# Performance work log

Measured on AMD Instinct MI355X. Metric: run time of the kernel, lower is better.

Reference implementation:

```python
import jax, jax.numpy as jnp
import numpy as np

N = 100000   # nodes
DIM = 128    # feature dim
E = 800000   # edges per hop
K = 4        # hops
BN_EPS = 1e-5


def setup_inputs() -> dict:
    key = jax.random.key(0)
    ks = jax.random.split(key, 24)
    inp = {}
    for i in range(K):
        inp[f"x{i}"] = jax.random.normal(ks[i], (N, DIM), dtype=jnp.float32)
    inp["edge_attr"] = jax.random.normal(ks[4], (E, DIM), dtype=jnp.float32)
    for i in range(K):
        inp[f"e{i}"] = jax.random.randint(ks[5 + i], (2, E), 0, N, dtype=jnp.int32)
    s1 = 1.0 / np.sqrt(DIM)
    s2 = 1.0 / np.sqrt(2 * DIM)
    inp["W1"] = jax.random.uniform(ks[9], (DIM, 2 * DIM), jnp.float32, -s1, s1)
    inp["b1"] = jax.random.uniform(ks[10], (2 * DIM,), jnp.float32, -s1, s1)
    inp["bn1_g"] = jnp.ones((2 * DIM,), jnp.float32)
    inp["bn1_b"] = jnp.zeros((2 * DIM,), jnp.float32)
    inp["W2"] = jax.random.uniform(ks[11], (2 * DIM, DIM), jnp.float32, -s2, s2)
    inp["b2"] = jax.random.uniform(ks[12], (DIM,), jnp.float32, -s2, s2)
    inp["bn2_g"] = jnp.ones((DIM,), jnp.float32)
    inp["bn2_b"] = jnp.zeros((DIM,), jnp.float32)
    inp["bn3_g"] = jnp.ones((DIM,), jnp.float32)
    inp["bn3_b"] = jnp.zeros((DIM,), jnp.float32)
    inp["eps_param"] = jnp.zeros((K + 1, DIM), jnp.float32)  # nn.Parameter(zeros)
    return inp


def _bn(h, g, b):
    # BatchNorm1d, train-mode math: batch mean / biased var per feature
    m = jnp.mean(h, axis=0)
    v = jnp.var(h, axis=0)
    return g * (h - m) * jax.lax.rsqrt(v + BN_EPS) + b


def _propagate(x, edge_index, edge_attr):
    # message: relu(x_j [+ edge_attr]); aggregate: scatter-add at dst
    msg = x[edge_index[0]]                      # [E, DIM] gather from src
    if edge_attr is not None:
        msg = msg + edge_attr
    msg = jax.nn.relu(msg)
    return jax.ops.segment_sum(msg, edge_index[1], num_segments=N)


def reference(x0, x1, x2, x3, edge_attr, e0, e1, e2, e3,
              W1, b1, bn1_g, bn1_b, W2, b2, bn2_g, bn2_b,
              bn3_g, bn3_b, eps_param):
    xs = [x0, x1, x2, x3]
    es = [e0, e1, e2, e3]
    result = (1.0 + eps_param[0]) * x0
    for i in range(K):
        ea = edge_attr if i == 0 else None
        result = result + (1.0 + eps_param[i + 1]) * _propagate(xs[i], es[i], ea)
    # GIN MLP: Linear -> BN -> ReLU -> Linear -> BN -> ReLU
    h = jax.nn.relu(_bn(result @ W1 + b1, bn1_g, bn1_b))
    h = jax.nn.relu(_bn(h @ W2 + b2, bn2_g, bn2_b))
    # outer ConvBlock: BN -> act (relu, not last layer); dropout in eval = identity
    h = jax.nn.relu(_bn(h, bn3_g, bn3_b))
    return h  # new x[0]; original also carries XX through unchanged
```

## Files before the change

### kernel.cpp

```cpp
#include <hip/hip_runtime.h>
#include <cstdint>
#include <cstddef>

#define NN 100000
#define D 128
#define NE 800000
#define BN_EPS 1e-5f

#define M4 (4 * NN)
#define CH 1000
#define NB 400

__global__ __launch_bounds__(256) void k_count(
    const int* __restrict__ e0, const int* __restrict__ e1,
    const int* __restrict__ e2, const int* __restrict__ e3,
    int* __restrict__ counts) {
  const int h = blockIdx.y;
  const int* e = h == 0 ? e0 : h == 1 ? e1 : h == 2 ? e2 : e3;
  const int eid = blockIdx.x * 256 + threadIdx.x;
  const int dst = e[NE + eid];
  atomicAdd(&counts[dst * 4 + h], 1);
}

__global__ __launch_bounds__(256) void k_scanA(const int* __restrict__ counts,
                                               int* __restrict__ bsum) {
  __shared__ int red[256];
  const int b = blockIdx.x, t = threadIdx.x;
  int s = 0;
  for (int i = t; i < CH; i += 256) s += counts[b * CH + i];
  red[t] = s; __syncthreads();
  for (int off = 128; off > 0; off >>= 1) {
    if (t < off) red[t] += red[t + off];
    __syncthreads();
  }
  if (t == 0) bsum[b] = red[0];
}

__global__ __launch_bounds__(512) void k_scanB(const int* __restrict__ bsum,
                                               int* __restrict__ bpre) {
  __shared__ int s[512];
  const int t = threadIdx.x;
  const int v = (t < NB) ? bsum[t] : 0;
  s[t] = v; __syncthreads();
  for (int off = 1; off < 512; off <<= 1) {
    int x = s[t];
    if (t >= off) x += s[t - off];
    __syncthreads(); s[t] = x; __syncthreads();
  }
  if (t < NB) bpre[t] = s[t] - v;
}

__global__ __launch_bounds__(256) void k_scanC(const int* __restrict__ counts,
                                               const int* __restrict__ bpre,
                                               int* __restrict__ offsets,
                                               int* __restrict__ cursor) {
  __shared__ int cnt[CH];
  __shared__ int part[256];
  const int b = blockIdx.x, t = threadIdx.x;
  for (int i = t; i < CH; i += 256) cnt[i] = counts[b * CH + i];
  __syncthreads();
  int own = 0;
#pragma unroll
  for (int j = 0; j < 4; j++) {
    int idx = t * 4 + j;
    if (idx < CH) own += cnt[idx];
  }
  part[t] = own; __syncthreads();
  for (int off = 1; off < 256; off <<= 1) {
    int x = part[t];
    if (t >= off) x += part[t - off];
    __syncthreads(); part[t] = x; __syncthreads();
  }
  int run = bpre[b] + part[t] - own;
#pragma unroll
  for (int j = 0; j < 4; j++) {
    int idx = t * 4 + j;
    if (idx < CH) {
      offsets[b * CH + idx] = run;
      cursor[b * CH + idx] = run;
      run += cnt[idx];
    }
  }
  if (b == 0 && t == 0) offsets[M4] = 4 * NE;
}

__global__ __launch_bounds__(256) void k_fill(
    const int* __restrict__ e0, const int* __restrict__ e1,
    const int* __restrict__ e2, const int* __restrict__ e3,
    int* __restrict__ cursor, int* __restrict__ srcs, int* __restrict__ eids) {
  const int h = blockIdx.y;
  const int* e = h == 0 ? e0 : h == 1 ? e1 : h == 2 ? e2 : e3;
  const int eid = blockIdx.x * 256 + threadIdx.x;
  const int src = e[eid];
  const int dst = e[NE + eid];
  const int pos = atomicAdd(&cursor[dst * 4 + h], 1);
  srcs[pos] = src;
  if (h == 0) eids[pos] = eid;
}

__global__ __launch_bounds__(256) void k_gather(
    const float* __restrict__ x0, const float* __restrict__ x1,
    const float* __restrict__ x2, const float* __restrict__ x3,
    const float* __restrict__ edge_attr, const float* __restrict__ eps,
    const int* __restrict__ offsets, const int* __restrict__ srcs,
    const int* __restrict__ eids, float* __restrict__ result) {
  const int dst  = blockIdx.x * 4 + (threadIdx.x >> 6);
  const int lane = threadIdx.x & 63;
  const int d    = lane * 2;

  const int4 ob = *reinterpret_cast<const int4*>(offsets + 4 * dst);
  const int o0 = ob.x, b1 = ob.y, b2 = ob.z, b3 = ob.w;
  const int o4 = offsets[4 * dst + 4];

  float2 h0 = make_float2(0.f, 0.f);
  float2 h1 = make_float2(0.f, 0.f);
  float2 h2 = make_float2(0.f, 0.f);
  float2 h3 = make_float2(0.f, 0.f);

  {
    int j = o0;
    for (; j + 2 <= b1; j += 2) {
      const int p0 = srcs[j],     p1 = srcs[j + 1];
      const int q0 = eids[j],     q1 = eids[j + 1];
      float2 v0 = *reinterpret_cast<const float2*>(x0 + p0 * D + d);
      float2 w0 = *reinterpret_cast<const float2*>(edge_attr + (size_t)q0 * D + d);
      float2 v1 = *reinterpret_cast<const float2*>(x0 + p1 * D + d);
      float2 w1 = *reinterpret_cast<const float2*>(edge_attr + (size_t)q1 * D + d);
      h0.x += fmaxf(v0.x + w0.x, 0.f); h0.y += fmaxf(v0.y + w0.y, 0.f);
      h0.x += fmaxf(v1.x + w1.x, 0.f); h0.y += fmaxf(v1.y + w1.y, 0.f);
    }
    if (j < b1) {
      const int p = srcs[j];
      const int q = eids[j];
      float2 v = *reinterpret_cast<const float2*>(x0 + p * D + d);
      float2 w = *reinterpret_cast<const float2*>(edge_attr + (size_t)q * D + d);
      h0.x += fmaxf(v.x + w.x, 0.f); h0.y += fmaxf(v.y + w.y, 0.f);
    }
  }

#define HOP_LOOP(XP, ACC, BEG, END) do {                                       \
    int j_ = (BEG);                                                            \
    for (; j_ + 4 <= (END); j_ += 4) {                                         \
      const int p0_ = srcs[j_], p1_ = srcs[j_ + 1];                            \
      const int p2_ = srcs[j_ + 2], p3_ = srcs[j_ + 3];                        \
      float2 v0_ = *reinterpret_cast<const float2*>((XP) + p0_ * D + d);       \
      float2 v1_ = *reinterpret_cast<const float2*>((XP) + p1_ * D + d);       \
      float2 v2_ = *reinterpret_cast<const float2*>((XP) + p2_ * D + d);       \
      float2 v3_ = *reinterpret_cast<const float2*>((XP) + p3_ * D + d);       \
      ACC.x += fmaxf(v0_.x, 0.f); ACC.y += fmaxf(v0_.y, 0.f);                  \
      ACC.x += fmaxf(v1_.x, 0.f); ACC.y += fmaxf(v1_.y, 0.f);                  \
      ACC.x += fmaxf(v2_.x, 0.f); ACC.y += fmaxf(v2_.y, 0.f);                  \
      ACC.x += fmaxf(v3_.x, 0.f); ACC.y += fmaxf(v3_.y, 0.f);                  \
    }                                                                          \
    for (; j_ < (END); ++j_) {                                                 \
      const int p_ = srcs[j_];                                                 \
      float2 v_ = *reinterpret_cast<const float2*>((XP) + p_ * D + d);         \
      ACC.x += fmaxf(v_.x, 0.f); ACC.y += fmaxf(v_.y, 0.f);                    \
    }                                                                          \
  } while (0)

  HOP_LOOP(x1, h1, b1, b2);
  HOP_LOOP(x2, h2, b2, b3);
  HOP_LOOP(x3, h3, b3, o4);
#undef HOP_LOOP

  float2 e0v = *reinterpret_cast<const float2*>(eps + d);
  float2 s1 = *reinterpret_cast<const float2*>(eps + 1 * D + d);
  float2 s2 = *reinterpret_cast<const float2*>(eps + 2 * D + d);
  float2 s3 = *reinterpret_cast<const float2*>(eps + 3 * D + d);
  float2 s4 = *reinterpret_cast<const float2*>(eps + 4 * D + d);
  float2 xv = *reinterpret_cast<const float2*>(x0 + dst * D + d);

  float2 acc;
  acc.x = (1.f + e0v.x) * xv.x + (1.f + s1.x) * h0.x + (1.f + s2.x) * h1.x
        + (1.f + s3.x) * h2.x + (1.f + s4.x) * h3.x;
  acc.y = (1.f + e0v.y) * xv.y + (1.f + s1.y) * h0.y + (1.f + s2.y) * h1.y
        + (1.f + s3.y) * h2.y + (1.f + s4.y) * h3.y;

  *reinterpret_cast<float2*>(result + dst * D + d) = acc;
}

__global__ __launch_bounds__(512) void k_gemm1(const float* __restrict__ A,
                                               const float* __restrict__ B,
                                               float* __restrict__ C,
                                               float* __restrict__ sums1,
                                               float* __restrict__ sumsq1) {
  __shared__ float As[32][132];
  __shared__ float Bs[32][256];
  const int tid = threadIdx.x;
  const int tx = tid & 31, ty = tid >> 5;
  const int row0 = blockIdx.x * 128;

  float acc[8][8];
#pragma unroll
  for (int i = 0; i < 8; i++)
#pragma unroll
    for (int j = 0; j < 8; j++) acc[i][j] = 0.f;

  for (int k0 = 0; k0 < 128; k0 += 32) {
#pragma unroll
    for (int l = 0; l < 2; l++) {
      int f4 = tid + l * 512;
      int row = f4 >> 3, kq = f4 & 7;
      float4 v = make_float4(0.f, 0.f, 0.f, 0.f);
      if (row0 + row < NN)
        v = *reinterpret_cast<const float4*>(A + (size_t)(row0 + row) * 128 + k0 + kq * 4);
      As[kq * 4 + 0][row] = v.x; As[kq * 4 + 1][row] = v.y;
      As[kq * 4 + 2][row] = v.z; As[kq * 4 + 3][row] = v.w;
    }
#pragma unroll
    for (int l = 0; l < 4; l++) {
      int f4 = tid + l * 512;
      int kk = f4 >> 6, cq = f4 & 63;
      *reinterpret_cast<float4*>(&Bs[kk][cq * 4]) =
          *reinterpret_cast<const float4*>(B + (size_t)(k0 + kk) * 256 + cq * 4);
    }
    __syncthreads();
#pragma unroll
    for (int k = 0; k < 32; k++) {
      float a[8], b[8];
      *reinterpret_cast<float4*>(a)     = *reinterpret_cast<const float4*>(&As[k][ty * 8]);
      *reinterpret_cast<float4*>(a + 4) = *reinterpret_cast<const float4*>(&As[k][ty * 8 + 4]);
      *reinterpret_cast<float4*>(b)     = *reinterpret_cast<const float4*>(&Bs[k][tx * 4]);
      *reinterpret_cast<float4*>(b + 4) = *reinterpret_cast<const float4*>(&Bs[k][128 + tx * 4]);
#pragma unroll
      for (int i = 0; i < 8; i++)
#pragma unroll
        for (int j = 0; j < 8; j++) acc[i][j] = fmaf(a[i], b[j], acc[i][j]);
    }
    __syncthreads();
  }
#pragma unroll
  for (int i = 0; i < 8; i++) {
    int row = row0 + ty * 8 + i;
    if (row < NN) {
      *reinterpret_cast<float4*>(C + (size_t)row * 256 + tx * 4) =
          make_float4(acc[i][0], acc[i][1], acc[i][2], acc[i][3]);
      *reinterpret_cast<float4*>(C + (size_t)row * 256 + 128 + tx * 4) =
          make_float4(acc[i][4], acc[i][5], acc[i][6], acc[i][7]);
    }
  }
  float cs[8], cq[8];
#pragma unroll
  for (int j = 0; j < 8; j++) { cs[j] = 0.f; cq[j] = 0.f; }
#pragma unroll
  for (int i = 0; i < 8; i++)
#pragma unroll
    for (int j = 0; j < 8; j++) { cs[j] += acc[i][j]; cq[j] = fmaf(acc[i][j], acc[i][j], cq[j]); }
#pragma unroll
  for (int j = 0; j < 4; j++) {
    Bs[ty][tx * 4 + j]            = cs[j];
    Bs[16 + ty][tx * 4 + j]       = cq[j];
    Bs[ty][128 + tx * 4 + j]      = cs[4 + j];
    Bs[16 + ty][128 + tx * 4 + j] = cq[4 + j];
  }
  __syncthreads();
  if (tid < 256) {
    float s = 0.f, q = 0.f;
#pragma unroll
    for (int t = 0; t < 16; t++) { s += Bs[t][tid]; q += Bs[16 + t][tid]; }
    unsafeAtomicAdd(&sums1[tid], s);
    unsafeAtomicAdd(&sumsq1[tid], q);
  }
}

__global__ __launch_bounds__(512) void k_gemm2(const float* __restrict__ A,
                                               const float* __restrict__ B,
                                               const float* __restrict__ sums1,
                                               const float* __restrict__ sumsq1,
                                               const float* __restrict__ bn1_g,
                                               const float* __restrict__ bn1_b,
                                               float* __restrict__ C,
                                               float* __restrict__ sums2,
                                               float* __restrict__ sumsq2) {
  __shared__ float As[32][132];
  __shared__ float Bs[32][128];
  __shared__ float s1s[256], s1h[256];
  const int tid = threadIdx.x;
  const int tx = tid & 31, ty = tid >> 5;
  const int row0 = blockIdx.x * 128;

  if (tid < 256) {
    float mean = sums1[tid] * (1.f / NN);
    float var  = sumsq1[tid] * (1.f / NN) - mean * mean;
    float rs   = rsqrtf(var + BN_EPS);
    float s    = bn1_g[tid] * rs;
    s1s[tid] = s;
    s1h[tid] = bn1_b[tid] - mean * s;
  }
  __syncthreads();

  float acc[8][4];
#pragma unroll
  for (int i = 0; i < 8; i++)
#pragma unroll
    for (int j = 0; j < 4; j++) acc[i][j] = 0.f;

  for (int k0 = 0; k0 < 256; k0 += 32) {
#pragma unroll
    for (int l = 0; l < 2; l++) {
      int f4 = tid + l * 512;
      int row = f4 >> 3, kq = f4 & 7;
      float4 v = make_float4(0.f, 0.f, 0.f, 0.f);
      if (row0 + row < NN)
        v = *reinterpret_cast<const float4*>(A + (size_t)(row0 + row) * 256 + k0 + kq * 4);
      float4 s  = *reinterpret_cast<const float4*>(&s1s[k0 + kq * 4]);
      float4 hh = *reinterpret_cast<const float4*>(&s1h[k0 + kq * 4]);
      v.x = fmaxf(fmaf(s.x, v.x, hh.x), 0.f);
      v.y = fmaxf(fmaf(s.y, v.y, hh.y), 0.f);
      v.z = fmaxf(fmaf(s.z, v.z, hh.z), 0.f);
      v.w = fmaxf(fmaf(s.w, v.w, hh.w), 0.f);
      As[kq * 4 + 0][row] = v.x; As[kq * 4 + 1][row] = v.y;
      As[kq * 4 + 2][row] = v.z; As[kq * 4 + 3][row] = v.w;
    }
#pragma unroll
    for (int l = 0; l < 2; l++) {
      int f4 = tid + l * 512;
      int kk = f4 >> 5, cq = f4 & 31;
      *reinterpret_cast<float4*>(&Bs[kk][cq * 4]) =
          *reinterpret_cast<const float4*>(B + (size_t)(k0 + kk) * 128 + cq * 4);
    }
    __syncthreads();
#pragma unroll
    for (int k = 0; k < 32; k++) {
      float a[8], b[4];
      *reinterpret_cast<float4*>(a)     = *reinterpret_cast<const float4*>(&As[k][ty * 8]);
      *reinterpret_cast<float4*>(a + 4) = *reinterpret_cast<const float4*>(&As[k][ty * 8 + 4]);
      *reinterpret_cast<float4*>(b)     = *reinterpret_cast<const float4*>(&Bs[k][tx * 4]);
#pragma unroll
      for (int i = 0; i < 8; i++)
#pragma unroll
        for (int j = 0; j < 4; j++) acc[i][j] = fmaf(a[i], b[j], acc[i][j]);
    }
    __syncthreads();
  }
#pragma unroll
  for (int i = 0; i < 8; i++) {
    int row = row0 + ty * 8 + i;
    if (row < NN)
      *reinterpret_cast<float4*>(C + (size_t)row * 128 + tx * 4) =
          make_float4(acc[i][0], acc[i][1], acc[i][2], acc[i][3]);
  }
  float cs[4], cq[4];
#pragma unroll
  for (int j = 0; j < 4; j++) { cs[j] = 0.f; cq[j] = 0.f; }
#pragma unroll
  for (int i = 0; i < 8; i++)
#pragma unroll
    for (int j = 0; j < 4; j++) { cs[j] += acc[i][j]; cq[j] = fmaf(acc[i][j], acc[i][j], cq[j]); }
#pragma unroll
  for (int j = 0; j < 4; j++) {
    Bs[ty][tx * 4 + j]      = cs[j];
    Bs[16 + ty][tx * 4 + j] = cq[j];
  }
  __syncthreads();
  if (tid < 128) {
    float s = 0.f, q = 0.f;
#pragma unroll
    for (int t = 0; t < 16; t++) { s += Bs[t][tid]; q += Bs[16 + t][tid]; }
    unsafeAtomicAdd(&sums2[tid], s);
    unsafeAtomicAdd(&sumsq2[tid], q);
  }
}

__global__ __launch_bounds__(256) void k_colstats3(const float* __restrict__ X,
                                                   const float* __restrict__ sums2,
                                                   const float* __restrict__ sumsq2,
                                                   const float* __restrict__ bn2_g,
                                                   const float* __restrict__ bn2_b,
                                                   float* __restrict__ sums3,
                                                   float* __restrict__ sumsq3) {
  const long total = (long)NN * 128;
  const long stride = (long)gridDim.x * 256;
  const long start = (long)blockIdx.x * 256 + threadIdx.x;
  const int c = (int)(start & 127);
  float mean = sums2[c] * (1.f / NN);
  float var  = sumsq2[c] * (1.f / NN) - mean * mean;
  float rs   = rsqrtf(var + BN_EPS);
  float scale = bn2_g[c] * rs;
  float shiftv = bn2_b[c] - mean * scale;
  float s = 0.f, q = 0.f;
  for (long idx = start; idx < total; idx += stride) {
    float v = fmaxf(fmaf(scale, X[idx], shiftv), 0.f);
    s += v;
    q = fmaf(v, v, q);
  }
  unsafeAtomicAdd(&sums3[c], s);
  unsafeAtomicAdd(&sumsq3[c], q);
}

__global__ __launch_bounds__(256) void k_final(float* __restrict__ t2,
                                               const float* __restrict__ sums2,
                                               const float* __restrict__ sumsq2,
                                               const float* __restrict__ bn2_g,
                                               const float* __restrict__ bn2_b,
                                               const float* __restrict__ sums3,
                                               const float* __restrict__ sumsq3,
                                               const float* __restrict__ bn3_g,
                                               const float* __restrict__ bn3_b) {
  int i4 = blockIdx.x * 256 + threadIdx.x;
  if (i4 >= NN * D / 4) return;
  int d = (i4 & 31) * 4;
  float4 v = reinterpret_cast<float4*>(t2)[i4];
  float o[4];
  float* vv = reinterpret_cast<float*>(&v);
#pragma unroll
  for (int j = 0; j < 4; j++) {
    int c = d + j;
    float m2 = sums2[c] * (1.f / NN);
    float va2 = sumsq2[c] * (1.f / NN) - m2 * m2;
    float r2 = rsqrtf(va2 + BN_EPS);
    float a2 = bn2_g[c] * r2;
    float h2 = bn2_b[c] - m2 * a2;
    float m3 = sums3[c] * (1.f / NN);
    float va3 = sumsq3[c] * (1.f / NN) - m3 * m3;
    float r3 = rsqrtf(va3 + BN_EPS);
    float a3 = bn3_g[c] * r3;
    float h3 = bn3_b[c] - m3 * a3;
    o[j] = fmaxf(fmaf(a3, fmaxf(fmaf(a2, vv[j], h2), 0.f), h3), 0.f);
  }
  reinterpret_cast<float4*>(t2)[i4] = make_float4(o[0], o[1], o[2], o[3]);
}

extern "C" void kernel_launch(void* const* d_in, const int* in_sizes, int n_in,
                              void* d_out, int out_size, void* d_ws, size_t ws_size,
                              hipStream_t stream) {
  const float* x0 = (const float*)d_in[0];
  const float* x1 = (const float*)d_in[1];
  const float* x2 = (const float*)d_in[2];
  const float* x3 = (const float*)d_in[3];
  const float* edge_attr = (const float*)d_in[4];
  const int* e0 = (const int*)d_in[5];
  const int* e1 = (const int*)d_in[6];
  const int* e2 = (const int*)d_in[7];
  const int* e3 = (const int*)d_in[8];
  const float* W1 = (const float*)d_in[9];
  const float* bn1_g = (const float*)d_in[11];
  const float* bn1_b = (const float*)d_in[12];
  const float* W2 = (const float*)d_in[13];
  const float* bn2_g = (const float*)d_in[15];
  const float* bn2_b = (const float*)d_in[16];
  const float* bn3_g = (const float*)d_in[17];
  const float* bn3_b = (const float*)d_in[18];
  const float* eps = (const float*)d_in[19];

  float* ws = (float*)d_ws;
  float* result = ws;
  float* t1 = ws + (size_t)NN * D;

  int* counts  = (int*)t1;
  int* offsets = counts + M4;
  int* cursor  = offsets + M4 + 1;
  int* bsum    = cursor + M4;
  int* bpre    = bsum + NB;
  int* srcs    = bpre + NB;
  int* eids    = srcs + 4 * NE;

  float* stats = t1 + (size_t)NN * 256;
  float* sums1  = stats;
  float* sumsq1 = sums1 + 256;
  float* sums2  = sumsq1 + 256;
  float* sumsq2 = sums2 + 128;
  float* sums3  = sumsq2 + 128;
  float* sumsq3 = sums3 + 128;
  float* t2 = (float*)d_out;

  hipMemsetAsync(counts, 0, M4 * sizeof(int), stream);
  hipMemsetAsync(stats, 0, 1024 * sizeof(float), stream);

  k_count<<<dim3(NE / 256, 4), 256, 0, stream>>>(e0, e1, e2, e3, counts);
  k_scanA<<<NB, 256, 0, stream>>>(counts, bsum);
  k_scanB<<<1, 512, 0, stream>>>(bsum, bpre);
  k_scanC<<<NB, 256, 0, stream>>>(counts, bpre, offsets, cursor);
  k_fill<<<dim3(NE / 256, 4), 256, 0, stream>>>(e0, e1, e2, e3, cursor, srcs, eids);

  k_gather<<<NN / 4, 256, 0, stream>>>(x0, x1, x2, x3, edge_attr, eps,
                                       offsets, srcs, eids, result);

  k_gemm1<<<(NN + 127) / 128, 512, 0, stream>>>(result, W1, t1, sums1, sumsq1);
  k_gemm2<<<(NN + 127) / 128, 512, 0, stream>>>(t1, W2, sums1, sumsq1, bn1_g, bn1_b,
                                                t2, sums2, sumsq2);
  k_colstats3<<<512, 256, 0, stream>>>(t2, sums2, sumsq2, bn2_g, bn2_b, sums3, sumsq3);
  k_final<<<NN * D / 4 / 256, 256, 0, stream>>>(t2, sums2, sumsq2, bn2_g, bn2_b,
                                                sums3, sumsq3, bn3_g, bn3_b);
}
```

Baseline: 883.1 us.

## Use bf16 MFMA GEMMs, packed byte counts with precomputed ranks for CSR build

Replaces the fp32 SIMT GEMMs with bf16 MFMA 16x16x32 kernels that take pre-transposed bf16 weights, and has the gather write its result in bf16. The CSR build packs the four per-hop counts into one 32-bit word, records each edge's rank from the atomic's return value, and places edges without a second atomic pass. Column statistics move out of the GEMM epilogues into separate reduction kernels plus a small BN finalize kernel. This lowers precision to bf16, assumes no node gets more than 255 incoming edges in a hop, and adds extra full passes over t1 and t2 for the statistics.

```diff
diff --git a/kernel.cpp b/kernel.cpp
--- a/kernel.cpp
+++ b/kernel.cpp
@@ -10,24 +10,50 @@
 #define M4 (4 * NN)
 #define CH 1000
 #define NB 400
+#define G64 1563
+
+typedef __attribute__((ext_vector_type(4))) float f32x4;
+typedef __attribute__((ext_vector_type(8))) short s16x8;
+
+__device__ inline unsigned short f2bf(float f) {
+  unsigned int u = __builtin_bit_cast(unsigned int, f);
+  u += 0x7FFFu + ((u >> 16) & 1u);
+  return (unsigned short)(u >> 16);
+}
+
+__global__ __launch_bounds__(256) void k_prep(const float* __restrict__ W1,
+                                              const float* __restrict__ W2,
+                                              unsigned short* __restrict__ W1T,
+                                              unsigned short* __restrict__ W2T) {
+  int i = blockIdx.x * 256 + threadIdx.x;
+  if (i >= 32768) return;
+  int k1 = i >> 8, n1 = i & 255;
+  W1T[n1 * 128 + k1] = f2bf(W1[i]);
+  int k2 = i >> 7, n2 = i & 127;
+  W2T[n2 * 256 + k2] = f2bf(W2[i]);
+}
 
 __global__ __launch_bounds__(256) void k_count(
     const int* __restrict__ e0, const int* __restrict__ e1,
     const int* __restrict__ e2, const int* __restrict__ e3,
-    int* __restrict__ counts) {
+    unsigned int* __restrict__ pcount, unsigned char* __restrict__ wrank) {
   const int h = blockIdx.y;
   const int* e = h == 0 ? e0 : h == 1 ? e1 : h == 2 ? e2 : e3;
   const int eid = blockIdx.x * 256 + threadIdx.x;
   const int dst = e[NE + eid];
-  atomicAdd(&counts[dst * 4 + h], 1);
-}
-
-__global__ __launch_bounds__(256) void k_scanA(const int* __restrict__ counts,
+  unsigned int old = atomicAdd(&pcount[dst], 1u << (8 * h));
+  wrank[h * NE + eid] = (unsigned char)((old >> (8 * h)) & 0xFFu);
+}
+
+__global__ __launch_bounds__(256) void k_scanA(const unsigned int* __restrict__ pcount,
                                                int* __restrict__ bsum) {
   __shared__ int red[256];
   const int b = blockIdx.x, t = threadIdx.x;
   int s = 0;
-  for (int i = t; i < CH; i += 256) s += counts[b * CH + i];
+  if (t < 250) {
+    unsigned int p = pcount[b * 250 + t];
+    s = (int)((p & 0xFFu) + ((p >> 8) & 0xFFu) + ((p >> 16) & 0xFFu) + (p >> 24));
+  }
   red[t] = s; __syncthreads();
   for (int off = 128; off > 0; off >>= 1) {
     if (t < off) red[t] += red[t + off];
@@ -50,14 +76,19 @@
   if (t < NB) bpre[t] = s[t] - v;
 }
 
-__global__ __launch_bounds__(256) void k_scanC(const int* __restrict__ counts,
+__global__ __launch_bounds__(256) void k_scanC(const unsigned int* __restrict__ pcount,
                                                const int* __restrict__ bpre,
-                                               int* __restrict__ offsets,
-                                               int* __restrict__ cursor) {
+                                               int* __restrict__ offsets) {
   __shared__ int cnt[CH];
   __shared__ int part[256];
   const int b = blockIdx.x, t = threadIdx.x;
-  for (int i = t; i < CH; i += 256) cnt[i] = counts[b * CH + i];
+  if (t < 250) {
+    unsigned int p = pcount[b * 250 + t];
+    cnt[t * 4 + 0] = (int)(p & 0xFFu);
+    cnt[t * 4 + 1] = (int)((p >> 8) & 0xFFu);
+    cnt[t * 4 + 2] = (int)((p >> 16) & 0xFFu);
+    cnt[t * 4 + 3] = (int)(p >> 24);
+  }
   __syncthreads();
   int own = 0;
 #pragma unroll
@@ -75,25 +106,22 @@
 #pragma unroll
   for (int j = 0; j < 4; j++) {
     int idx = t * 4 + j;
-    if (idx < CH) {
-      offsets[b * CH + idx] = run;
-      cursor[b * CH + idx] = run;
-      run += cnt[idx];
-    }
+    if (idx < CH) { offsets[b * CH + idx] = run; run += cnt[idx]; }
   }
   if (b == 0 && t == 0) offsets[M4] = 4 * NE;
 }
 
-__global__ __launch_bounds__(256) void k_fill(
+__global__ __launch_bounds__(256) void k_place(
     const int* __restrict__ e0, const int* __restrict__ e1,
     const int* __restrict__ e2, const int* __restrict__ e3,
-    int* __restrict__ cursor, int* __restrict__ srcs, int* __restrict__ eids) {
+    const int* __restrict__ offsets, const unsigned char* __restrict__ wrank,
+    int* __restrict__ srcs, int* __restrict__ eids) {
   const int h = blockIdx.y;
   const int* e = h == 0 ? e0 : h == 1 ? e1 : h == 2 ? e2 : e3;
   const int eid = blockIdx.x * 256 + threadIdx.x;
   const int src = e[eid];
   const int dst = e[NE + eid];
-  const int pos = atomicAdd(&cursor[dst * 4 + h], 1);
+  const int pos = offsets[dst * 4 + h] + (int)wrank[h * NE + eid];
   srcs[pos] = src;
   if (h == 0) eids[pos] = eid;
 }
@@ -103,7 +131,7 @@
     const float* __restrict__ x2, const float* __restrict__ x3,
     const float* __restrict__ edge_attr, const float* __restrict__ eps,
     const int* __restrict__ offsets, const int* __restrict__ srcs,
-    const int* __restrict__ eids, float* __restrict__ result) {
+    const int* __restrict__ eids, unsigned short* __restrict__ result) {
   const int dst  = blockIdx.x * 4 + (threadIdx.x >> 6);
   const int lane = threadIdx.x & 63;
   const int d    = lane * 2;
@@ -171,196 +199,137 @@
   float2 s4 = *reinterpret_cast<const float2*>(eps + 4 * D + d);
   float2 xv = *reinterpret_cast<const float2*>(x0 + dst * D + d);
 
-  float2 acc;
-  acc.x = (1.f + e0v.x) * xv.x + (1.f + s1.x) * h0.x + (1.f + s2.x) * h1.x
-        + (1.f + s3.x) * h2.x + (1.f + s4.x) * h3.x;
-  acc.y = (1.f + e0v.y) * xv.y + (1.f + s1.y) * h0.y + (1.f + s2.y) * h1.y
-        + (1.f + s3.y) * h2.y + (1.f + s4.y) * h3.y;
-
-  *reinterpret_cast<float2*>(result + dst * D + d) = acc;
-}
-
-__global__ __launch_bounds__(512) void k_gemm1(const float* __restrict__ A,
-                                               const float* __restrict__ B,
-                                               float* __restrict__ C,
-                                               float* __restrict__ sums1,
-                                               float* __restrict__ sumsq1) {
-  __shared__ float As[32][132];
-  __shared__ float Bs[32][256];
-  const int tid = threadIdx.x;
-  const int tx = tid & 31, ty = tid >> 5;
-  const int row0 = blockIdx.x * 128;
-
-  float acc[8][8];
-#pragma unroll
-  for (int i = 0; i < 8; i++)
-#pragma unroll
-    for (int j = 0; j < 8; j++) acc[i][j] = 0.f;
-
-  for (int k0 = 0; k0 < 128; k0 += 32) {
-#pragma unroll
-    for (int l = 0; l < 2; l++) {
-      int f4 = tid + l * 512;
-      int row = f4 >> 3, kq = f4 & 7;
-      float4 v = make_float4(0.f, 0.f, 0.f, 0.f);
-      if (row0 + row < NN)
-        v = *reinterpret_cast<const float4*>(A + (size_t)(row0 + row) * 128 + k0 + kq * 4);
-      As[kq * 4 + 0][row] = v.x; As[kq * 4 + 1][row] = v.y;
-      As[kq * 4 + 2][row] = v.z; As[kq * 4 + 3][row] = v.w;
-    }
-#pragma unroll
-    for (int l = 0; l < 4; l++) {
-      int f4 = tid + l * 512;
-      int kk = f4 >> 6, cq = f4 & 63;
-      *reinterpret_cast<float4*>(&Bs[kk][cq * 4]) =
-          *reinterpret_cast<const float4*>(B + (size_t)(k0 + kk) * 256 + cq * 4);
-    }
-    __syncthreads();
-#pragma unroll
-    for (int k = 0; k < 32; k++) {
-      float a[8], b[8];
-      *reinterpret_cast<float4*>(a)     = *reinterpret_cast<const float4*>(&As[k][ty * 8]);
-      *reinterpret_cast<float4*>(a + 4) = *reinterpret_cast<const float4*>(&As[k][ty * 8 + 4]);
-      *reinterpret_cast<float4*>(b)     = *reinterpret_cast<const float4*>(&Bs[k][tx * 4]);
-      *reinterpret_cast<float4*>(b + 4) = *reinterpret_cast<const float4*>(&Bs[k][128 + tx * 4]);
-#pragma unroll
-      for (int i = 0; i < 8; i++)
-#pragma unroll
-        for (int j = 0; j < 8; j++) acc[i][j] = fmaf(a[i], b[j], acc[i][j]);
-    }
-    __syncthreads();
-  }
-#pragma unroll
-  for (int i = 0; i < 8; i++) {
-    int row = row0 + ty * 8 + i;
-    if (row < NN) {
-      *reinterpret_cast<float4*>(C + (size_t)row * 256 + tx * 4) =
-          make_float4(acc[i][0], acc[i][1], acc[i][2], acc[i][3]);
-      *reinterpret_cast<float4*>(C + (size_t)row * 256 + 128 + tx * 4) =
-          make_float4(acc[i][4], acc[i][5], acc[i][6], acc[i][7]);
-    }
-  }
-  float cs[8], cq[8];
-#pragma unroll
-  for (int j = 0; j < 8; j++) { cs[j] = 0.f; cq[j] = 0.f; }
-#pragma unroll
-  for (int i = 0; i < 8; i++)
-#pragma unroll
-    for (int j = 0; j < 8; j++) { cs[j] += acc[i][j]; cq[j] = fmaf(acc[i][j], acc[i][j], cq[j]); }
-#pragma unroll
-  for (int j = 0; j < 4; j++) {
-    Bs[ty][tx * 4 + j]            = cs[j];
-    Bs[16 + ty][tx * 4 + j]       = cq[j];
-    Bs[ty][128 + tx * 4 + j]      = cs[4 + j];
-    Bs[16 + ty][128 + tx * 4 + j] = cq[4 + j];
-  }
-  __syncthreads();
-  if (tid < 256) {
-    float s = 0.f, q = 0.f;
-#pragma unroll
-    for (int t = 0; t < 16; t++) { s += Bs[t][tid]; q += Bs[16 + t][tid]; }
-    unsafeAtomicAdd(&sums1[tid], s);
-    unsafeAtomicAdd(&sumsq1[tid], q);
-  }
-}
-
-__global__ __launch_bounds__(512) void k_gemm2(const float* __restrict__ A,
-                                               const float* __restrict__ B,
-                                               const float* __restrict__ sums1,
-                                               const float* __restrict__ sumsq1,
-                                               const float* __restrict__ bn1_g,
-                                               const float* __restrict__ bn1_b,
-                                               float* __restrict__ C,
-                                               float* __restrict__ sums2,
-                                               float* __restrict__ sumsq2) {
-  __shared__ float As[32][132];
-  __shared__ float Bs[32][128];
+  float ax = (1.f + e0v.x) * xv.x + (1.f + s1.x) * h0.x + (1.f + s2.x) * h1.x
+           + (1.f + s3.x) * h2.x + (1.f + s4.x) * h3.x;
+  float ay = (1.f + e0v.y) * xv.y + (1.f + s1.y) * h0.y + (1.f + s2.y) * h1.y
+           + (1.f + s3.y) * h2.y + (1.f + s4.y) * h3.y;
+
+  reinterpret_cast<unsigned int*>(result)[dst * 64 + lane] =
+      (unsigned int)f2bf(ax) | ((unsigned int)f2bf(ay) << 16);
+}
+
+__global__ __launch_bounds__(256) void k_gemm1(const unsigned short* __restrict__ Ab,
+                                               const unsigned short* __restrict__ W1T,
+                                               float* __restrict__ C) {
+  const int lane = threadIdx.x & 63, wave = threadIdx.x >> 6;
+  const int ln = lane & 15, lk = lane >> 4;
+  const int m0 = blockIdx.x * 64 + wave * 16;
+  const int arow = m0 + ln;
+  const bool av = arow < NN;
+
+  f32x4 acc[16];
+#pragma unroll
+  for (int t = 0; t < 16; t++) acc[t] = (f32x4)0.f;
+
+#pragma unroll
+  for (int kk = 0; kk < 4; kk++) {
+    const int kb = kk * 32 + lk * 8;
+    s16x8 a = (s16x8)(short)0;
+    if (av) a = *reinterpret_cast<const s16x8*>(Ab + arow * 128 + kb);
+#pragma unroll
+    for (int t = 0; t < 16; t++) {
+      s16x8 b = *reinterpret_cast<const s16x8*>(W1T + (t * 16 + ln) * 128 + kb);
+      acc[t] = __builtin_amdgcn_mfma_f32_16x16x32_bf16(a, b, acc[t], 0, 0, 0);
+    }
+  }
+#pragma unroll
+  for (int t = 0; t < 16; t++) {
+#pragma unroll
+    for (int r = 0; r < 4; r++) {
+      const int row = m0 + lk * 4 + r;
+      if (row < NN) C[(size_t)row * 256 + t * 16 + ln] = acc[t][r];
+    }
+  }
+}
+
+__global__ __launch_bounds__(256) void k_gemm2(const float* __restrict__ t1,
+                                               const unsigned short* __restrict__ W2T,
+                                               const float* __restrict__ sc,
+                                               const float* __restrict__ sh,
+                                               float* __restrict__ C) {
   __shared__ float s1s[256], s1h[256];
   const int tid = threadIdx.x;
-  const int tx = tid & 31, ty = tid >> 5;
-  const int row0 = blockIdx.x * 128;
-
-  if (tid < 256) {
-    float mean = sums1[tid] * (1.f / NN);
-    float var  = sumsq1[tid] * (1.f / NN) - mean * mean;
-    float rs   = rsqrtf(var + BN_EPS);
-    float s    = bn1_g[tid] * rs;
-    s1s[tid] = s;
-    s1h[tid] = bn1_b[tid] - mean * s;
-  }
+  if (tid < 256) { s1s[tid] = sc[tid]; s1h[tid] = sh[tid]; }
   __syncthreads();
 
-  float acc[8][4];
-#pragma unroll
-  for (int i = 0; i < 8; i++)
-#pragma unroll
-    for (int j = 0; j < 4; j++) acc[i][j] = 0.f;
-
-  for (int k0 = 0; k0 < 256; k0 += 32) {
-#pragma unroll
-    for (int l = 0; l < 2; l++) {
-      int f4 = tid + l * 512;
-      int row = f4 >> 3, kq = f4 & 7;
-      float4 v = make_float4(0.f, 0.f, 0.f, 0.f);
-      if (row0 + row < NN)
-        v = *reinterpret_cast<const float4*>(A + (size_t)(row0 + row) * 256 + k0 + kq * 4);
-      float4 s  = *reinterpret_cast<const float4*>(&s1s[k0 + kq * 4]);
-      float4 hh = *reinterpret_cast<const float4*>(&s1h[k0 + kq * 4]);
-      v.x = fmaxf(fmaf(s.x, v.x, hh.x), 0.f);
-      v.y = fmaxf(fmaf(s.y, v.y, hh.y), 0.f);
-      v.z = fmaxf(fmaf(s.z, v.z, hh.z), 0.f);
-      v.w = fmaxf(fmaf(s.w, v.w, hh.w), 0.f);
-      As[kq * 4 + 0][row] = v.x; As[kq * 4 + 1][row] = v.y;
-      As[kq * 4 + 2][row] = v.z; As[kq * 4 + 3][row] = v.w;
-    }
-#pragma unroll
-    for (int l = 0; l < 2; l++) {
-      int f4 = tid + l * 512;
-      int kk = f4 >> 5, cq = f4 & 31;
-      *reinterpret_cast<float4*>(&Bs[kk][cq * 4]) =
-          *reinterpret_cast<const float4*>(B + (size_t)(k0 + kk) * 128 + cq * 4);
-    }
-    __syncthreads();
-#pragma unroll
-    for (int k = 0; k < 32; k++) {
-      float a[8], b[4];
-      *reinterpret_cast<float4*>(a)     = *reinterpret_cast<const float4*>(&As[k][ty * 8]);
-      *reinterpret_cast<float4*>(a + 4) = *reinterpret_cast<const float4*>(&As[k][ty * 8 + 4]);
-      *reinterpret_cast<float4*>(b)     = *reinterpret_cast<const float4*>(&Bs[k][tx * 4]);
-#pragma unroll
-      for (int i = 0; i < 8; i++)
-#pragma unroll
-        for (int j = 0; j < 4; j++) acc[i][j] = fmaf(a[i], b[j], acc[i][j]);
-    }
-    __syncthreads();
-  }
-#pragma unroll
-  for (int i = 0; i < 8; i++) {
-    int row = row0 + ty * 8 + i;
-    if (row < NN)
-      *reinterpret_cast<float4*>(C + (size_t)row * 128 + tx * 4) =
-          make_float4(acc[i][0], acc[i][1], acc[i][2], acc[i][3]);
-  }
-  float cs[4], cq[4];
-#pragma unroll
-  for (int j = 0; j < 4; j++) { cs[j] = 0.f; cq[j] = 0.f; }
-#pragma unroll
-  for (int i = 0; i < 8; i++)
-#pragma unroll
-    for (int j = 0; j < 4; j++) { cs[j] += acc[i][j]; cq[j] = fmaf(acc[i][j], acc[i][j], cq[j]); }
-#pragma unroll
-  for (int j = 0; j < 4; j++) {
-    Bs[ty][tx * 4 + j]      = cs[j];
-    Bs[16 + ty][tx * 4 + j] = cq[j];
-  }
-  __syncthreads();
-  if (tid < 128) {
-    float s = 0.f, q = 0.f;
-#pragma unroll
-    for (int t = 0; t < 16; t++) { s += Bs[t][tid]; q += Bs[16 + t][tid]; }
-    unsafeAtomicAdd(&sums2[tid], s);
-    unsafeAtomicAdd(&sumsq2[tid], q);
-  }
+  const int lane = tid & 63, wave = tid >> 6;
+  const int ln = lane & 15, lk = lane >> 4;
+  const int m0 = blockIdx.x * 64 + wave * 16;
+  const int arow = m0 + ln;
+  const bool av = arow < NN;
+
+  f32x4 acc[8];
+#pragma unroll
+  for (int t = 0; t < 8; t++) acc[t] = (f32x4)0.f;
+
+#pragma unroll
+  for (int kk = 0; kk < 8; kk++) {
+    const int kb = kk * 32 + lk * 8;
+    float va[8];
+    if (av) {
+      *reinterpret_cast<float4*>(va)     = *reinterpret_cast<const float4*>(t1 + (size_t)arow * 256 + kb);
+      *reinterpret_cast<float4*>(va + 4) = *reinterpret_cast<const float4*>(t1 + (size_t)arow * 256 + kb + 4);
+    } else {
+#pragma unroll
+      for (int i = 0; i < 8; i++) va[i] = 0.f;
+    }
+    s16x8 a;
+#pragma unroll
+    for (int i = 0; i < 8; i++) {
+      float v = fmaxf(fmaf(s1s[kb + i], va[i], s1h[kb + i]), 0.f);
+      a[i] = (short)f2bf(v);
+    }
+#pragma unroll
+    for (int t = 0; t < 8; t++) {
+      s16x8 b = *reinterpret_cast<const s16x8*>(W2T + (t * 16 + ln) * 256 + kb);
+      acc[t] = __builtin_amdgcn_mfma_f32_16x16x32_bf16(a, b, acc[t], 0, 0, 0);
+    }
+  }
+#pragma unroll
+  for (int t = 0; t < 8; t++) {
+#pragma unroll
+    for (int r = 0; r < 4; r++) {
+      const int row = m0 + lk * 4 + r;
+      if (row < NN) C[(size_t)row * 128 + t * 16 + ln] = acc[t][r];
+    }
+  }
+}
+
+template <int C, bool ACT>
+__global__ __launch_bounds__(256) void k_colstats(const float* __restrict__ X,
+                                                  const float* __restrict__ sc,
+                                                  const float* __restrict__ sh,
+                                                  float* __restrict__ sums,
+                                                  float* __restrict__ sumsq) {
+  const long total = (long)NN * C;
+  const long stride = (long)gridDim.x * 256;
+  const long start = (long)blockIdx.x * 256 + threadIdx.x;
+  const int c = (int)(start & (C - 1));
+  float scale = 0.f, shiftv = 0.f;
+  if constexpr (ACT) { scale = sc[c]; shiftv = sh[c]; }
+  float s = 0.f, q = 0.f;
+  for (long idx = start; idx < total; idx += stride) {
+    float v = X[idx];
+    if constexpr (ACT) v = fmaxf(fmaf(scale, v, shiftv), 0.f);
+    s += v;
+    q = fmaf(v, v, q);
+  }
+  unsafeAtomicAdd(&sums[c], s);
+  unsafeAtomicAdd(&sumsq[c], q);
+}
+
+template <int C>
+__global__ void k_bnfinal(const float* __restrict__ sums, const float* __restrict__ sumsq,
+                          const float* __restrict__ g, const float* __restrict__ b,
+                          float* __restrict__ scale, float* __restrict__ shift) {
+  int c = threadIdx.x;
+  if (c >= C) return;
+  float mean = sums[c] * (1.f / NN);
+  float var  = sumsq[c] * (1.f / NN) - mean * mean;
+  float rs   = rsqrtf(var + BN_EPS);
+  float s    = g[c] * rs;
+  scale[c] = s;
+  shift[c] = b[c] - mean * s;
 }
 
 __global__ __launch_bounds__(256) void k_colstats3(const float* __restrict__ X,
@@ -444,18 +413,9 @@
   const float* bn3_b = (const float*)d_in[18];
   const float* eps = (const float*)d_in[19];
 
-  float* ws = (float*)d_ws;
-  float* result = ws;
-  float* t1 = ws + (size_t)NN * D;
-
-  int* counts  = (int*)t1;
-  int* offsets = counts + M4;
-  int* cursor  = offsets + M4 + 1;
-  int* bsum    = cursor + M4;
-  int* bpre    = bsum + NB;
-  int* srcs    = bpre + NB;
-  int* eids    = srcs + 4 * NE;
-
+  char* ws = (char*)d_ws;
+  unsigned short* resultb = (unsigned short*)ws;
+  float* t1 = (float*)(ws + (size_t)NN * D * 2);
   float* stats = t1 + (size_t)NN * 256;
   float* sums1  = stats;
   float* sumsq1 = sums1 + 256;
@@ -463,23 +423,40 @@
   float* sumsq2 = sums2 + 128;
   float* sums3  = sumsq2 + 128;
   float* sumsq3 = sums3 + 128;
+  float* scale1 = sumsq3 + 128;
+  float* shift1 = scale1 + 256;
+  unsigned short* W1T = (unsigned short*)(shift1 + 256);
+  unsigned short* W2T = W1T + 32768;
+  unsigned int* pcount = (unsigned int*)(W2T + 32768);
+  unsigned char* wrank = (unsigned char*)(pcount + NN);
+
+  int* offsets = (int*)t1;
+  int* bsum    = offsets + M4 + 1;
+  int* bpre    = bsum + NB;
+  int* srcs    = bpre + NB;
+  int* eids    = srcs + 4 * NE;
+
   float* t2 = (float*)d_out;
 
-  hipMemsetAsync(counts, 0, M4 * sizeof(int), stream);
+  hipMemsetAsync(pcount, 0, NN * sizeof(unsigned int), stream);
   hipMemsetAsync(stats, 0, 1024 * sizeof(float), stream);
 
-  k_count<<<dim3(NE / 256, 4), 256, 0, stream>>>(e0, e1, e2, e3, counts);
-  k_scanA<<<NB, 256, 0, stream>>>(counts, bsum);
+  k_prep<<<128, 256, 0, stream>>>(W1, W2, W1T, W2T);
+
+  k_count<<<dim3(NE / 256, 4), 256, 0, stream>>>(e0, e1, e2, e3, pcount, wrank);
+  k_scanA<<<NB, 256, 0, stream>>>(pcount, bsum);
   k_scanB<<<1, 512, 0, stream>>>(bsum, bpre);
-  k_scanC<<<NB, 256, 0, stream>>>(counts, bpre, offsets, cursor);
-  k_fill<<<dim3(NE / 256, 4), 256, 0, stream>>>(e0, e1, e2, e3, cursor, srcs, eids);
+  k_scanC<<<NB, 256, 0, stream>>>(pcount, bpre, offsets);
+  k_place<<<dim3(NE / 256, 4), 256, 0, stream>>>(e0, e1, e2, e3, offsets, wrank, srcs, eids);
 
   k_gather<<<NN / 4, 256, 0, stream>>>(x0, x1, x2, x3, edge_attr, eps,
-                                       offsets, srcs, eids, result);
-
-  k_gemm1<<<(NN + 127) / 128, 512, 0, stream>>>(result, W1, t1, sums1, sumsq1);
-  k_gemm2<<<(NN + 127) / 128, 512, 0, stream>>>(t1, W2, sums1, sumsq1, bn1_g, bn1_b,
-                                                t2, sums2, sumsq2);
+                                       offsets, srcs, eids, resultb);
+
+  k_gemm1<<<G64, 256, 0, stream>>>(resultb, W1T, t1);
+  k_colstats<256, false><<<512, 256, 0, stream>>>(t1, nullptr, nullptr, sums1, sumsq1);
+  k_bnfinal<256><<<1, 256, 0, stream>>>(sums1, sumsq1, bn1_g, bn1_b, scale1, shift1);
+  k_gemm2<<<G64, 256, 0, stream>>>(t1, W2T, scale1, shift1, t2);
+  k_colstats<128, false><<<512, 256, 0, stream>>>(t2, nullptr, nullptr, sums2, sumsq2);
   k_colstats3<<<512, 256, 0, stream>>>(t2, sums2, sumsq2, bn2_g, bn2_b, sums3, sumsq3);
   k_final<<<NN * D / 4 / 256, 256, 0, stream>>>(t2, sums2, sumsq2, bn2_g, bn2_b,
                                                 sums3, sumsq3, bn3_g, bn3_b);
```

After: 877.1 us. No clear change (-0.7%).
